# Performance work log

Hardware: AMD Instinct MI355X
Metric: run time of the kernel (lower is better)

## Reference

```python
import jax, jax.numpy as jnp
import numpy as np

N_QUBITS = 10
BATCH = 16384
Q_DEPTH = 2


def _apply_1q_shared(state, U, q):
    # state: [B, 2, 2, ..., 2]; U: [2, 2] complex, acting on wire q
    state = jnp.moveaxis(state, 1 + q, -1)
    state = jnp.einsum('b...i,ji->b...j', state, U)
    return jnp.moveaxis(state, -1, 1 + q)


def _apply_ry_batched(state, angles, q):
    # per-sample RY(angle) on wire q; angles: [B] float
    c = jnp.cos(angles * 0.5).astype(jnp.complex64)
    s = jnp.sin(angles * 0.5).astype(jnp.complex64)
    U = jnp.stack([jnp.stack([c, -s], -1), jnp.stack([s, c], -1)], -2)  # [B,2,2]
    state = jnp.moveaxis(state, 1 + q, -1)
    state = jnp.einsum('b...i,bji->b...j', state, U)
    return jnp.moveaxis(state, -1, 1 + q)


def _rot_matrix(phi, theta, omega):
    # PennyLane Rot = RZ(omega) @ RY(theta) @ RZ(phi)
    c = jnp.cos(theta * 0.5)
    s = jnp.sin(theta * 0.5)
    m00 = jnp.exp(-0.5j * (phi + omega)) * c
    m01 = -jnp.exp(0.5j * (phi - omega)) * s
    m10 = jnp.exp(-0.5j * (phi - omega)) * s
    m11 = jnp.exp(0.5j * (phi + omega)) * c
    return jnp.stack([jnp.stack([m00, m01]), jnp.stack([m10, m11])]).astype(jnp.complex64)


def _apply_cnot(state, c, t):
    st = jnp.moveaxis(state, (1 + c, 1 + t), (1, 2))  # [B, ctrl, tgt, ...]
    st = jnp.stack([st[:, 0], st[:, 1, ::-1]], axis=1)  # flip target where ctrl=1
    return jnp.moveaxis(st, (1, 2), (1 + c, 1 + t))


def setup_inputs() -> dict:
    key = jax.random.key(0)
    k1, k2 = jax.random.split(key)
    x = jax.random.uniform(k1, (BATCH, N_QUBITS), dtype=jnp.float32) * np.pi
    q_weights = 0.01 * jax.random.normal(k2, (Q_DEPTH, N_QUBITS, 3), dtype=jnp.float32)
    return {"x": x, "q_weights": q_weights}


def reference(x, q_weights) -> jnp.ndarray:
    B, n = x.shape
    L = q_weights.shape[0]
    # |0...0> statevector, batched: [B] + [2]*n (axis q <-> wire q, wire 0 most significant)
    state = jnp.zeros((B, 2 ** n), jnp.complex64).at[:, 0].set(1.0)
    state = state.reshape((B,) + (2,) * n)
    # AngleEmbedding(rotation='Y')
    for q in range(n):
        state = _apply_ry_batched(state, x[:, q], q)
    # StronglyEntanglingLayers: Rot on each wire, then ring of CNOTs with range (l % (n-1)) + 1
    for l in range(L):
        for q in range(n):
            U = _rot_matrix(q_weights[l, q, 0], q_weights[l, q, 1], q_weights[l, q, 2])
            state = _apply_1q_shared(state, U, q)
        r = (l % (n - 1)) + 1
        for q in range(n):
            state = _apply_cnot(state, q, (q + r) % n)
    probs = jnp.abs(state.reshape(B, 2 ** n)) ** 2  # [B, 2^n]
    bits = (np.arange(2 ** n)[:, None] >> (n - 1 - np.arange(n))[None, :]) & 1
    signs = jnp.asarray(1.0 - 2.0 * bits, jnp.float32)  # [2^n, n], PauliZ eigenvalues
    return (probs @ signs).astype(jnp.float32)  # [B, n] expvals
```

## Files before the change

### kernel.cpp

```cpp
#include <hip/hip_runtime.h>

#define DEVINL __device__ __forceinline__

struct GC { int laneXor, regXor, rowL, rowR; };
struct Circ { GC g[20]; int sgnL[10], sgnR[10]; };

constexpr Circ build_circ() {
    Circ c{};
    unsigned A[10] = {};
    for (int i = 0; i < 10; ++i) A[i] = 1u << i;
    for (int w = 0; w < 10; ++w) {
        int pos = 9 - w;
        unsigned m = 1u << pos;
        c.g[w] = GC{ int(m >> 4), int(m & 15u), int(m >> 4), int(m & 15u) };
    }
    for (int q = 0; q < 10; ++q) { int pc = 9 - q, pt = 9 - ((q + 1) % 10); A[pt] ^= A[pc]; }
    unsigned M[10] = {}, Inv[10] = {};
    for (int i = 0; i < 10; ++i) { M[i] = A[i]; Inv[i] = 1u << i; }
    for (int col = 0; col < 10; ++col) {
        int piv = col;
        while (!((M[piv] >> col) & 1u)) ++piv;
        unsigned tm = M[col]; M[col] = M[piv]; M[piv] = tm;
        unsigned ti = Inv[col]; Inv[col] = Inv[piv]; Inv[piv] = ti;
        for (int r = 0; r < 10; ++r)
            if (r != col && ((M[r] >> col) & 1u)) { M[r] ^= M[col]; Inv[r] ^= Inv[col]; }
    }
    for (int w = 0; w < 10; ++w) {
        int pos = 9 - w;
        unsigned m = 0;
        for (int i = 0; i < 10; ++i) m |= ((Inv[i] >> pos) & 1u) << i;
        unsigned row = A[pos];
        c.g[10 + w] = GC{ int(m >> 4), int(m & 15u), int(row >> 4), int(row & 15u) };
    }
    for (int q = 0; q < 10; ++q) { int pc = 9 - q, pt = 9 - ((q + 2) % 10); A[pt] ^= A[pc]; }
    for (int q = 0; q < 10; ++q) { unsigned row = A[9 - q]; c.sgnL[q] = int(row >> 4); c.sgnR[q] = int(row & 15u); }
    return c;
}

constexpr Circ CC = build_circ();

static_assert(CC.g[10].rowL == 31 && CC.g[10].rowR == 15, "w0 row");
static_assert(CC.g[11].rowL == 48 && CC.g[11].rowR == 0,  "w1 row");
static_assert(CC.g[12].rowL == 56 && CC.g[12].rowR == 0,  "w2 row");
static_assert(CC.g[13].rowL == 60 && CC.g[13].rowR == 0,  "w3 row");
static_assert(CC.g[14].rowL == 62 && CC.g[14].rowR == 0,  "w4 row");
static_assert(CC.g[15].rowL == 63 && CC.g[15].rowR == 0,  "w5 row");
static_assert(CC.g[16].rowL == 63 && CC.g[16].rowR == 8,  "w6 row");
static_assert(CC.g[17].rowL == 63 && CC.g[17].rowR == 12, "w7 row");
static_assert(CC.g[18].rowL == 63 && CC.g[18].rowR == 14, "w8 row");
static_assert(CC.g[19].rowL == 63 && CC.g[19].rowR == 15, "w9 row");

DEVINL float csw(float v, int sw) {
    return __int_as_float(__float_as_int(v) ^ sw);
}

template<int XOR>
DEVINL float lx(float v, int lane) {
    int x = __float_as_int(v);
    int r;
    if constexpr (XOR < 32) r = __builtin_amdgcn_ds_swizzle(x, 0x1F | (XOR << 10));
    else                    r = __builtin_amdgcn_ds_bpermute((lane ^ XOR) << 2, x);
    return __int_as_float(r);
}

DEVINL void wf(const float* sm, float xw, int w,
               float& a0r, float& a0i, float& a1r, float& a1i) {
    float h = 0.5f * xw;
    float s = __sinf(h), c = __cosf(h);
    float m0 = sm[w * 4 + 0], m1 = sm[w * 4 + 1], m2 = sm[w * 4 + 2], m3 = sm[w * 4 + 3];
    a0r =  m0 * c + m2 * s;
    a0i =  m1 * c + m3 * s;
    a1r = -m2 * c + m0 * s;
    a1i =  m3 * c - m1 * s;
}

template<int G>
DEVINL void rygates(float (&ar)[16], float (&ai)[16], const float* sm, int lane,
                    const int (&sw)[10]) {
    if constexpr (G < 20) {
        constexpr GC gc = CC.g[G];
        constexpr int w = G - 10;
        float t  = sm[40 + w * 4 + 1];
        float tt = csw(t, sw[w]);
        float br_[16], bi_[16];
        if constexpr (gc.laneXor == 0) {
            #pragma unroll
            for (int r = 0; r < 16; ++r) { br_[r] = ar[r ^ gc.regXor]; bi_[r] = ai[r ^ gc.regXor]; }
        } else {
            #pragma unroll
            for (int r = 0; r < 16; ++r) {
                br_[r] = lx<gc.laneXor>(ar[r ^ gc.regXor], lane);
                bi_[r] = lx<gc.laneXor>(ai[r ^ gc.regXor], lane);
            }
        }
        #pragma unroll
        for (int r = 0; r < 16; ++r) {
            const bool sR = __builtin_popcount(unsigned(gc.rowR & r)) & 1;
            if (sR) { ar[r] = fmaf( tt, br_[r], ar[r]); ai[r] = fmaf( tt, bi_[r], ai[r]); }
            else    { ar[r] = fmaf(-tt, br_[r], ar[r]); ai[r] = fmaf(-tt, bi_[r], ai[r]); }
        }
        rygates<G + 1>(ar, ai, sm, lane, sw);
    }
}

__global__ __launch_bounds__(256) void qsim(const float* __restrict__ x,
                                            const float* __restrict__ qw,
                                            float* __restrict__ out, int B) {
    __shared__ float sm[80];
    {
        int g = threadIdx.x;
        if (g < 10) {
            float phi = qw[g * 3 + 0], th = qw[g * 3 + 1], om = qw[g * 3 + 2];
            float c = cosf(0.5f * th), s = sinf(0.5f * th);
            float apo = 0.5f * (phi + om), amo = 0.5f * (phi - om);
            sm[g * 4 + 0] =  cosf(apo) * c;
            sm[g * 4 + 1] = -sinf(apo) * c;
            sm[g * 4 + 2] = -cosf(amo) * s;
            sm[g * 4 + 3] = -sinf(amo) * s;
        } else if (g < 20) {
            int w = g - 10;
            float phi = qw[g * 3 + 0], th = qw[g * 3 + 1];
            float c = cosf(0.5f * th), s = sinf(0.5f * th);
            sm[40 + w * 4 + 0] = c;
            sm[40 + w * 4 + 1] = s / c;
            sm[40 + w * 4 + 2] = cosf(0.5f * phi);
            sm[40 + w * 4 + 3] = -sinf(0.5f * phi);
        }
    }
    __syncthreads();

    int lane = threadIdx.x & 63;
    int b = __builtin_amdgcn_readfirstlane(blockIdx.x * 4 + (threadIdx.x >> 6));
    if (b >= B) return;
    const float* xb = x + b * 10;

    int l = lane;
    int p48 = (l >> 4) ^ (l >> 5);
    int p56 = p48 ^ (l >> 3);
    int p60 = p56 ^ (l >> 2);
    int p62 = p60 ^ (l >> 1);
    int p63 = p62 ^ l;
    int p31 = p63 ^ (l >> 5);
    int s48 = p48 << 31, s56 = p56 << 31, s60 = p60 << 31;
    int s62 = p62 << 31, s63 = p63 << 31, s31 = p31 << 31;
    int sw[10] = { s31, s48, s56, s60, s62, s63, s63, s63, s63, s63 };

    float t01r[4], t01i[4], t23r[4], t23i[4];
    {
        float a0r, a0i, a1r, a1i, b0r, b0i, b1r, b1i;
        wf(sm, xb[9], 9, a0r, a0i, a1r, a1i);
        wf(sm, xb[8], 8, b0r, b0i, b1r, b1i);
        t01r[0] = a0r * b0r - a0i * b0i;  t01i[0] = a0r * b0i + a0i * b0r;
        t01r[1] = a1r * b0r - a1i * b0i;  t01i[1] = a1r * b0i + a1i * b0r;
        t01r[2] = a0r * b1r - a0i * b1i;  t01i[2] = a0r * b1i + a0i * b1r;
        t01r[3] = a1r * b1r - a1i * b1i;  t01i[3] = a1r * b1i + a1i * b1r;
        wf(sm, xb[7], 7, a0r, a0i, a1r, a1i);
        wf(sm, xb[6], 6, b0r, b0i, b1r, b1i);
        t23r[0] = a0r * b0r - a0i * b0i;  t23i[0] = a0r * b0i + a0i * b0r;
        t23r[1] = a1r * b0r - a1i * b0i;  t23i[1] = a1r * b0i + a1i * b0r;
        t23r[2] = a0r * b1r - a0i * b1i;  t23i[2] = a0r * b1i + a0i * b1r;
        t23r[3] = a1r * b1r - a1i * b1i;  t23i[3] = a1r * b1i + a1i * b1r;
    }

    float lfr, lfi;
    {
        float ear = sm[40 + 1 * 4 + 2], eai = csw(sm[40 + 1 * 4 + 3], sw[1]);
        #pragma unroll
        for (int w = 2; w <= 5; ++w) {
            float er = sm[40 + w * 4 + 2], ei = csw(sm[40 + w * 4 + 3], sw[w]);
            float nr = ear * er - eai * ei;
            float ni = ear * ei + eai * er;
            ear = nr; eai = ni;
        }
        float sc = sm[40];
        #pragma unroll
        for (int w = 1; w < 10; ++w) sc *= sm[40 + w * 4];
        lfr = ear * sc; lfi = eai * sc;
        #pragma unroll
        for (int jj = 0; jj < 6; ++jj) {
            int w = 5 - jj;
            float a0r, a0i, a1r, a1i;
            wf(sm, xb[w], w, a0r, a0i, a1r, a1i);
            int bit = (lane >> jj) & 1;
            float pr = bit ? a1r : a0r;
            float pi = bit ? a1i : a0i;
            float nr = lfr * pr - lfi * pi;
            float ni = lfr * pi + lfi * pr;
            lfr = nr; lfi = ni;
        }
    }

    float e6r = sm[40 + 6 * 4 + 2], e6i = csw(sm[40 + 6 * 4 + 3], sw[6]);
    float e7r = sm[40 + 7 * 4 + 2], e7i = csw(sm[40 + 7 * 4 + 3], sw[7]);
    float Pr_ = e6r * e7r - e6i * e7i, Pi_ = e6r * e7i + e6i * e7r;
    float Qr_ = e6r * e7r + e6i * e7i, Qi_ = e6i * e7r - e6r * e7i;
    float t23pr[4], t23pi[4];
    t23pr[0] = t23r[0] * Pr_ - t23i[0] * Pi_;  t23pi[0] = t23r[0] * Pi_ + t23i[0] * Pr_;
    t23pr[1] = t23r[1] * Qr_ - t23i[1] * Qi_;  t23pi[1] = t23r[1] * Qi_ + t23i[1] * Qr_;
    t23pr[2] = t23r[2] * Pr_ + t23i[2] * Pi_;  t23pi[2] = t23i[2] * Pr_ - t23r[2] * Pi_;
    t23pr[3] = t23r[3] * Qr_ + t23i[3] * Qi_;  t23pi[3] = t23i[3] * Qr_ - t23r[3] * Qi_;

    float e0r = sm[40 + 0 * 4 + 2], e0i = csw(sm[40 + 0 * 4 + 3], sw[0]);
    float e9r = sm[40 + 9 * 4 + 2], e9i = csw(sm[40 + 9 * 4 + 3], sw[9]);
    float e8r = sm[40 + 8 * 4 + 2], e8i = csw(sm[40 + 8 * 4 + 3], sw[8]);
    float ebr = e0r * e9r - e0i * e9i, ebi = e0r * e9i + e0i * e9r;
    float G0r = e8r * ebr - e8i * ebi, G0i = e8r * ebi + e8i * ebr;
    float G1r = e8r * ebr + e8i * ebi, G1i = e8i * ebr - e8r * ebi;

    float g4r[4], g4i[4];
    #pragma unroll
    for (int v = 0; v < 4; ++v) {
        g4r[v] = lfr * t01r[v] - lfi * t01i[v];
        g4i[v] = lfr * t01i[v] + lfi * t01r[v];
    }
    float ar[16], ai[16];
    #pragma unroll
    for (int r = 0; r < 16; ++r) {
        float tr = g4r[r & 3] * t23pr[r >> 2] - g4i[r & 3] * t23pi[r >> 2];
        float ti = g4r[r & 3] * t23pi[r >> 2] + g4i[r & 3] * t23pr[r >> 2];
        float gr = (r & 1) ? G1r : G0r;
        float gi = (r & 1) ? G1i : G0i;
        if (__builtin_popcount(unsigned(r & 14)) & 1) gi = -gi;
        ar[r] = tr * gr - ti * gi;
        ai[r] = tr * gi + ti * gr;
    }

    rygates<10>(ar, ai, sm, lane, sw);

    float wv[16];
    #pragma unroll
    for (int r = 0; r < 16; ++r) wv[r] = ar[r] * ar[r] + ai[r] * ai[r];
    #pragma unroll
    for (int bS = 1; bS < 16; bS <<= 1) {
        #pragma unroll
        for (int r = 0; r < 16; ++r) {
            if (!(r & bS)) {
                float xv = wv[r], yv = wv[r | bS];
                wv[r]      = xv + yv;
                wv[r | bS] = xv - yv;
            }
        }
    }

    float e[10];
    #pragma unroll
    for (int q = 0; q < 10; ++q) {
        int slq = __popc(unsigned(lane & CC.sgnL[q])) & 1;
        e[q] = csw(wv[CC.sgnR[q]], slq << 31);
    }
    #pragma unroll
    for (int q = 0; q < 10; ++q) {
        e[q] += lx<1>(e[q], lane);
        e[q] += lx<2>(e[q], lane);
        e[q] += lx<4>(e[q], lane);
        e[q] += lx<8>(e[q], lane);
        e[q] += lx<16>(e[q], lane);
        e[q] += lx<32>(e[q], lane);
    }
    float v = e[0];
    #pragma unroll
    for (int q = 1; q < 10; ++q) v = (lane == q) ? e[q] : v;
    if (lane < 10) out[b * 10 + lane] = v;
}

extern "C" void kernel_launch(void* const* d_in, const int* in_sizes, int n_in,
                              void* d_out, int out_size, void* d_ws, size_t ws_size,
                              hipStream_t stream) {
    const float* x  = (const float*)d_in[0];
    const float* qw = (const float*)d_in[1];
    float* out = (float*)d_out;
    int B = in_sizes[0] / 10;
    int blocks = (B + 3) / 4;
    hipLaunchKernelGGL(qsim, dim3(blocks), dim3(256), 0, stream, x, qw, out, B);
}
```

Baseline: 91.06 us.

## Split weight prep into separate kernel, use DPP/permlane shuffles and packed gate math

Moves the per-block trig precomputation of weight-derived constants into a tiny prep kernel writing a global constant table, removing the shared-memory setup and block barrier from the main kernel. Replaces ds_swizzle/bpermute cross-lane exchanges with DPP quad permutes and permlane16/32 swaps where available. Packs real/imag amplitudes into 2-wide float vectors for packed FMA, reorders the RY gate applications, and trims the final Walsh transform and wave reduction by packing the ten outputs into grouped lanes. It adds a second kernel launch and relies on global-memory constant loads instead of LDS.

```diff
diff --git a/kernel.cpp b/kernel.cpp
--- a/kernel.cpp
+++ b/kernel.cpp
@@ -1,6 +1,8 @@
 #include <hip/hip_runtime.h>
 
 #define DEVINL __device__ __forceinline__
+
+typedef float f32x2 __attribute__((ext_vector_type(2)));
 
 struct GC { int laneXor, regXor, rowL, rowR; };
 struct Circ { GC g[20]; int sgnL[10], sgnR[10]; };
@@ -49,86 +51,136 @@
 static_assert(CC.g[17].rowL == 63 && CC.g[17].rowR == 12, "w7 row");
 static_assert(CC.g[18].rowL == 63 && CC.g[18].rowR == 14, "w8 row");
 static_assert(CC.g[19].rowL == 63 && CC.g[19].rowR == 15, "w9 row");
+static_assert(CC.g[10].laneXor == 48 && CC.g[10].regXor == 0, "w0 m");
+static_assert(CC.g[11].laneXor == 24 && CC.g[12].laneXor == 12, "w1/w2 m");
+static_assert(CC.g[13].laneXor == 6  && CC.g[14].laneXor == 3,  "w3/w4 m");
+static_assert(CC.g[15].laneXor == 1  && CC.g[15].regXor == 8,   "w5 m");
+static_assert(CC.g[16].laneXor == 0 && CC.g[16].regXor == 12, "w6 m");
+static_assert(CC.g[17].laneXor == 0 && CC.g[17].regXor == 6,  "w7 m");
+static_assert(CC.g[18].laneXor == 0 && CC.g[18].regXor == 3,  "w8 m");
+static_assert(CC.g[19].laneXor == 48 && CC.g[19].regXor == 1,   "w9 m");
+
+#if __has_builtin(__builtin_amdgcn_permlane32_swap)
+#define HAS_PL32 1
+#else
+#define HAS_PL32 0
+#endif
+#if __has_builtin(__builtin_amdgcn_permlane16_swap)
+#define HAS_PL16 1
+#else
+#define HAS_PL16 0
+#endif
 
 DEVINL float csw(float v, int sw) {
     return __int_as_float(__float_as_int(v) ^ sw);
 }
 
+DEVINL float xor32_val(float v, int lane) {
+#if HAS_PL32
+    auto r = __builtin_amdgcn_permlane32_swap(__float_as_int(v), __float_as_int(v), false, false);
+    return (__int_as_float(r[0]) + __int_as_float(r[1])) - v;
+#else
+    return __int_as_float(__builtin_amdgcn_ds_bpermute((lane ^ 32) << 2, __float_as_int(v)));
+#endif
+}
+DEVINL float xor48_val(float v, int lane) {
+#if HAS_PL32 && HAS_PL16
+    float t = xor32_val(v, lane);
+    auto r = __builtin_amdgcn_permlane16_swap(__float_as_int(t), __float_as_int(t), false, false);
+    return (__int_as_float(r[0]) + __int_as_float(r[1])) - t;
+#else
+    return __int_as_float(__builtin_amdgcn_ds_bpermute((lane ^ 48) << 2, __float_as_int(v)));
+#endif
+}
+DEVINL float bsum16(float v, int lane) {
+#if HAS_PL16
+    auto r = __builtin_amdgcn_permlane16_swap(__float_as_int(v), __float_as_int(v), false, false);
+    return __int_as_float(r[0]) + __int_as_float(r[1]);
+#else
+    return v + __int_as_float(__builtin_amdgcn_ds_swizzle(__float_as_int(v), 0x1F | (16 << 10)));
+#endif
+}
+DEVINL float bsum32(float v, int lane) {
+#if HAS_PL32
+    auto r = __builtin_amdgcn_permlane32_swap(__float_as_int(v), __float_as_int(v), false, false);
+    return __int_as_float(r[0]) + __int_as_float(r[1]);
+#else
+    return v + __int_as_float(__builtin_amdgcn_ds_bpermute((lane ^ 32) << 2, __float_as_int(v)));
+#endif
+}
+
 template<int XOR>
-DEVINL float lx(float v, int lane) {
-    int x = __float_as_int(v);
-    int r;
-    if constexpr (XOR < 32) r = __builtin_amdgcn_ds_swizzle(x, 0x1F | (XOR << 10));
-    else                    r = __builtin_amdgcn_ds_bpermute((lane ^ XOR) << 2, x);
-    return __int_as_float(r);
-}
-
-DEVINL void wf(const float* sm, float xw, int w,
+DEVINL float fetch(float v, int lane) {
+    if constexpr (XOR == 0)      return v;
+    else if constexpr (XOR == 1) return __int_as_float(__builtin_amdgcn_update_dpp(0, __float_as_int(v), 0xB1, 0xF, 0xF, true));
+    else if constexpr (XOR == 2) return __int_as_float(__builtin_amdgcn_update_dpp(0, __float_as_int(v), 0x4E, 0xF, 0xF, true));
+    else if constexpr (XOR == 3) return __int_as_float(__builtin_amdgcn_update_dpp(0, __float_as_int(v), 0x1B, 0xF, 0xF, true));
+    else if constexpr (XOR == 32) return xor32_val(v, lane);
+    else if constexpr (XOR == 48) return xor48_val(v, lane);
+    else if constexpr (XOR < 32) return __int_as_float(__builtin_amdgcn_ds_swizzle(__float_as_int(v), 0x1F | (XOR << 10)));
+    else return __int_as_float(__builtin_amdgcn_ds_bpermute((lane ^ XOR) << 2, __float_as_int(v)));
+}
+
+__device__ __attribute__((aligned(16))) float g_cst[80];
+
+__global__ void qprep(const float* __restrict__ qw) {
+    int g = threadIdx.x;
+    if (g < 10) {
+        float phi = qw[g * 3 + 0], th = qw[g * 3 + 1], om = qw[g * 3 + 2];
+        float c = cosf(0.5f * th), s = sinf(0.5f * th);
+        float apo = 0.5f * (phi + om), amo = 0.5f * (phi - om);
+        g_cst[g * 4 + 0] =  cosf(apo) * c;
+        g_cst[g * 4 + 1] = -sinf(apo) * c;
+        g_cst[g * 4 + 2] = -cosf(amo) * s;
+        g_cst[g * 4 + 3] = -sinf(amo) * s;
+    } else if (g < 20) {
+        int w = g - 10;
+        float phi = qw[g * 3 + 0], th = qw[g * 3 + 1];
+        float c = cosf(0.5f * th), s = sinf(0.5f * th);
+        g_cst[40 + w] = s / c;
+        g_cst[50 + w * 2 + 0] =  cosf(0.5f * phi);
+        g_cst[50 + w * 2 + 1] = -sinf(0.5f * phi);
+    } else if (g == 20) {
+        float p = 1.f;
+        for (int w = 0; w < 10; ++w) p *= cosf(0.5f * qw[(10 + w) * 3 + 1]);
+        g_cst[70] = p;
+    }
+}
+
+DEVINL void wf(const float* cst, float xw, int w,
                float& a0r, float& a0i, float& a1r, float& a1i) {
     float h = 0.5f * xw;
     float s = __sinf(h), c = __cosf(h);
-    float m0 = sm[w * 4 + 0], m1 = sm[w * 4 + 1], m2 = sm[w * 4 + 2], m3 = sm[w * 4 + 3];
+    float m0 = cst[w * 4 + 0], m1 = cst[w * 4 + 1], m2 = cst[w * 4 + 2], m3 = cst[w * 4 + 3];
     a0r =  m0 * c + m2 * s;
     a0i =  m1 * c + m3 * s;
     a1r = -m2 * c + m0 * s;
     a1i =  m3 * c - m1 * s;
 }
 
-template<int G>
-DEVINL void rygates(float (&ar)[16], float (&ai)[16], const float* sm, int lane,
-                    const int (&sw)[10]) {
-    if constexpr (G < 20) {
-        constexpr GC gc = CC.g[G];
-        constexpr int w = G - 10;
-        float t  = sm[40 + w * 4 + 1];
-        float tt = csw(t, sw[w]);
-        float br_[16], bi_[16];
-        if constexpr (gc.laneXor == 0) {
-            #pragma unroll
-            for (int r = 0; r < 16; ++r) { br_[r] = ar[r ^ gc.regXor]; bi_[r] = ai[r ^ gc.regXor]; }
-        } else {
-            #pragma unroll
-            for (int r = 0; r < 16; ++r) {
-                br_[r] = lx<gc.laneXor>(ar[r ^ gc.regXor], lane);
-                bi_[r] = lx<gc.laneXor>(ai[r ^ gc.regXor], lane);
-            }
-        }
-        #pragma unroll
-        for (int r = 0; r < 16; ++r) {
-            const bool sR = __builtin_popcount(unsigned(gc.rowR & r)) & 1;
-            if (sR) { ar[r] = fmaf( tt, br_[r], ar[r]); ai[r] = fmaf( tt, bi_[r], ai[r]); }
-            else    { ar[r] = fmaf(-tt, br_[r], ar[r]); ai[r] = fmaf(-tt, bi_[r], ai[r]); }
-        }
-        rygates<G + 1>(ar, ai, sm, lane, sw);
+template<int W>
+DEVINL void apply_gate(f32x2 (&a2)[16], const float* cst, int lane, const int (&sw)[10]) {
+    constexpr GC gc = CC.g[10 + W];
+    float tt = csw(cst[40 + W], sw[W]);
+    f32x2 tv; tv.x = tt; tv.y = tt;
+    f32x2 b2[16];
+    #pragma unroll
+    for (int r = 0; r < 16; ++r) {
+        f32x2 s = a2[r ^ gc.regXor];
+        b2[r].x = fetch<gc.laneXor>(s.x, lane);
+        b2[r].y = fetch<gc.laneXor>(s.y, lane);
+    }
+    #pragma unroll
+    for (int r = 0; r < 16; ++r) {
+        const bool sR = __builtin_popcount(unsigned(gc.rowR & r)) & 1;
+        if (sR) a2[r] = a2[r] + tv * b2[r];
+        else    a2[r] = a2[r] - tv * b2[r];
     }
 }
 
 __global__ __launch_bounds__(256) void qsim(const float* __restrict__ x,
-                                            const float* __restrict__ qw,
                                             float* __restrict__ out, int B) {
-    __shared__ float sm[80];
-    {
-        int g = threadIdx.x;
-        if (g < 10) {
-            float phi = qw[g * 3 + 0], th = qw[g * 3 + 1], om = qw[g * 3 + 2];
-            float c = cosf(0.5f * th), s = sinf(0.5f * th);
-            float apo = 0.5f * (phi + om), amo = 0.5f * (phi - om);
-            sm[g * 4 + 0] =  cosf(apo) * c;
-            sm[g * 4 + 1] = -sinf(apo) * c;
-            sm[g * 4 + 2] = -cosf(amo) * s;
-            sm[g * 4 + 3] = -sinf(amo) * s;
-        } else if (g < 20) {
-            int w = g - 10;
-            float phi = qw[g * 3 + 0], th = qw[g * 3 + 1];
-            float c = cosf(0.5f * th), s = sinf(0.5f * th);
-            sm[40 + w * 4 + 0] = c;
-            sm[40 + w * 4 + 1] = s / c;
-            sm[40 + w * 4 + 2] = cosf(0.5f * phi);
-            sm[40 + w * 4 + 3] = -sinf(0.5f * phi);
-        }
-    }
-    __syncthreads();
-
+    const float* cst = g_cst;
     int lane = threadIdx.x & 63;
     int b = __builtin_amdgcn_readfirstlane(blockIdx.x * 4 + (threadIdx.x >> 6));
     if (b >= B) return;
@@ -148,14 +200,14 @@
     float t01r[4], t01i[4], t23r[4], t23i[4];
     {
         float a0r, a0i, a1r, a1i, b0r, b0i, b1r, b1i;
-        wf(sm, xb[9], 9, a0r, a0i, a1r, a1i);
-        wf(sm, xb[8], 8, b0r, b0i, b1r, b1i);
+        wf(cst, xb[9], 9, a0r, a0i, a1r, a1i);
+        wf(cst, xb[8], 8, b0r, b0i, b1r, b1i);
         t01r[0] = a0r * b0r - a0i * b0i;  t01i[0] = a0r * b0i + a0i * b0r;
         t01r[1] = a1r * b0r - a1i * b0i;  t01i[1] = a1r * b0i + a1i * b0r;
         t01r[2] = a0r * b1r - a0i * b1i;  t01i[2] = a0r * b1i + a0i * b1r;
         t01r[3] = a1r * b1r - a1i * b1i;  t01i[3] = a1r * b1i + a1i * b1r;
-        wf(sm, xb[7], 7, a0r, a0i, a1r, a1i);
-        wf(sm, xb[6], 6, b0r, b0i, b1r, b1i);
+        wf(cst, xb[7], 7, a0r, a0i, a1r, a1i);
+        wf(cst, xb[6], 6, b0r, b0i, b1r, b1i);
         t23r[0] = a0r * b0r - a0i * b0i;  t23i[0] = a0r * b0i + a0i * b0r;
         t23r[1] = a1r * b0r - a1i * b0i;  t23i[1] = a1r * b0i + a1i * b0r;
         t23r[2] = a0r * b1r - a0i * b1i;  t23i[2] = a0r * b1i + a0i * b1r;
@@ -164,23 +216,21 @@
 
     float lfr, lfi;
     {
-        float ear = sm[40 + 1 * 4 + 2], eai = csw(sm[40 + 1 * 4 + 3], sw[1]);
+        float ear = cst[50 + 1 * 2], eai = csw(cst[50 + 1 * 2 + 1], sw[1]);
         #pragma unroll
         for (int w = 2; w <= 5; ++w) {
-            float er = sm[40 + w * 4 + 2], ei = csw(sm[40 + w * 4 + 3], sw[w]);
+            float er = cst[50 + w * 2], ei = csw(cst[50 + w * 2 + 1], sw[w]);
             float nr = ear * er - eai * ei;
             float ni = ear * ei + eai * er;
             ear = nr; eai = ni;
         }
-        float sc = sm[40];
-        #pragma unroll
-        for (int w = 1; w < 10; ++w) sc *= sm[40 + w * 4];
+        float sc = cst[70];
         lfr = ear * sc; lfi = eai * sc;
         #pragma unroll
         for (int jj = 0; jj < 6; ++jj) {
             int w = 5 - jj;
             float a0r, a0i, a1r, a1i;
-            wf(sm, xb[w], w, a0r, a0i, a1r, a1i);
+            wf(cst, xb[w], w, a0r, a0i, a1r, a1i);
             int bit = (lane >> jj) & 1;
             float pr = bit ? a1r : a0r;
             float pi = bit ? a1i : a0i;
@@ -190,8 +240,8 @@
         }
     }
 
-    float e6r = sm[40 + 6 * 4 + 2], e6i = csw(sm[40 + 6 * 4 + 3], sw[6]);
-    float e7r = sm[40 + 7 * 4 + 2], e7i = csw(sm[40 + 7 * 4 + 3], sw[7]);
+    float e6r = cst[50 + 6 * 2], e6i = csw(cst[50 + 6 * 2 + 1], sw[6]);
+    float e7r = cst[50 + 7 * 2], e7i = csw(cst[50 + 7 * 2 + 1], sw[7]);
     float Pr_ = e6r * e7r - e6i * e7i, Pi_ = e6r * e7i + e6i * e7r;
     float Qr_ = e6r * e7r + e6i * e7i, Qi_ = e6i * e7r - e6r * e7i;
     float t23pr[4], t23pi[4];
@@ -200,9 +250,9 @@
     t23pr[2] = t23r[2] * Pr_ + t23i[2] * Pi_;  t23pi[2] = t23i[2] * Pr_ - t23r[2] * Pi_;
     t23pr[3] = t23r[3] * Qr_ + t23i[3] * Qi_;  t23pi[3] = t23i[3] * Qr_ - t23r[3] * Qi_;
 
-    float e0r = sm[40 + 0 * 4 + 2], e0i = csw(sm[40 + 0 * 4 + 3], sw[0]);
-    float e9r = sm[40 + 9 * 4 + 2], e9i = csw(sm[40 + 9 * 4 + 3], sw[9]);
-    float e8r = sm[40 + 8 * 4 + 2], e8i = csw(sm[40 + 8 * 4 + 3], sw[8]);
+    float e0r = cst[50 + 0 * 2], e0i = csw(cst[50 + 0 * 2 + 1], sw[0]);
+    float e9r = cst[50 + 9 * 2], e9i = csw(cst[50 + 9 * 2 + 1], sw[9]);
+    float e8r = cst[50 + 8 * 2], e8i = csw(cst[50 + 8 * 2 + 1], sw[8]);
     float ebr = e0r * e9r - e0i * e9i, ebi = e0r * e9i + e0i * e9r;
     float G0r = e8r * ebr - e8i * ebi, G0i = e8r * ebi + e8i * ebr;
     float G1r = e8r * ebr + e8i * ebi, G1i = e8i * ebr - e8r * ebi;
@@ -213,7 +263,7 @@
         g4r[v] = lfr * t01r[v] - lfi * t01i[v];
         g4i[v] = lfr * t01i[v] + lfi * t01r[v];
     }
-    float ar[16], ai[16];
+    f32x2 a2[16];
     #pragma unroll
     for (int r = 0; r < 16; ++r) {
         float tr = g4r[r & 3] * t23pr[r >> 2] - g4i[r & 3] * t23pi[r >> 2];
@@ -221,17 +271,26 @@
         float gr = (r & 1) ? G1r : G0r;
         float gi = (r & 1) ? G1i : G0i;
         if (__builtin_popcount(unsigned(r & 14)) & 1) gi = -gi;
-        ar[r] = tr * gr - ti * gi;
-        ai[r] = tr * gi + ti * gr;
-    }
-
-    rygates<10>(ar, ai, sm, lane, sw);
+        a2[r].x = tr * gr - ti * gi;
+        a2[r].y = tr * gi + ti * gr;
+    }
+
+    apply_gate<1>(a2, cst, lane, sw);
+    apply_gate<4>(a2, cst, lane, sw);
+    apply_gate<2>(a2, cst, lane, sw);
+    apply_gate<5>(a2, cst, lane, sw);
+    apply_gate<3>(a2, cst, lane, sw);
+    apply_gate<6>(a2, cst, lane, sw);
+    apply_gate<0>(a2, cst, lane, sw);
+    apply_gate<7>(a2, cst, lane, sw);
+    apply_gate<9>(a2, cst, lane, sw);
+    apply_gate<8>(a2, cst, lane, sw);
 
     float wv[16];
     #pragma unroll
-    for (int r = 0; r < 16; ++r) wv[r] = ar[r] * ar[r] + ai[r] * ai[r];
-    #pragma unroll
-    for (int bS = 1; bS < 16; bS <<= 1) {
+    for (int r = 0; r < 16; ++r) wv[r] = a2[r].x * a2[r].x + a2[r].y * a2[r].y;
+    #pragma unroll
+    for (int bS = 1; bS < 8; bS <<= 1) {
         #pragma unroll
         for (int r = 0; r < 16; ++r) {
             if (!(r & bS)) {
@@ -245,22 +304,37 @@
     float e[10];
     #pragma unroll
     for (int q = 0; q < 10; ++q) {
+        const int R = CC.sgnR[q];
+        float num = (R & 8) ? (wv[R ^ 8] - wv[R]) : (wv[R] + wv[R ^ 8]);
         int slq = __popc(unsigned(lane & CC.sgnL[q])) & 1;
-        e[q] = csw(wv[CC.sgnR[q]], slq << 31);
-    }
+        e[q] = csw(num, slq << 31);
+    }
+
     #pragma unroll
     for (int q = 0; q < 10; ++q) {
-        e[q] += lx<1>(e[q], lane);
-        e[q] += lx<2>(e[q], lane);
-        e[q] += lx<4>(e[q], lane);
-        e[q] += lx<8>(e[q], lane);
-        e[q] += lx<16>(e[q], lane);
-        e[q] += lx<32>(e[q], lane);
-    }
-    float v = e[0];
-    #pragma unroll
-    for (int q = 1; q < 10; ++q) v = (lane == q) ? e[q] : v;
-    if (lane < 10) out[b * 10 + lane] = v;
+        e[q] += fetch<1>(e[q], lane);
+        e[q] += fetch<2>(e[q], lane);
+    }
+    int s = lane & 3;
+    bool s1 = (s & 1) != 0, s2 = (s & 2) != 0;
+    float v0 = s1 ? e[1] : e[0];
+    float u0 = s1 ? e[3] : e[2];
+    v0 = s2 ? u0 : v0;
+    float v1 = s1 ? e[5] : e[4];
+    float u1 = s1 ? e[7] : e[6];
+    v1 = s2 ? u1 : v1;
+    float v2 = s1 ? e[9] : e[8];
+
+    v0 += fetch<4>(v0, lane);  v1 += fetch<4>(v1, lane);  v2 += fetch<4>(v2, lane);
+    v0 += fetch<8>(v0, lane);  v1 += fetch<8>(v1, lane);  v2 += fetch<8>(v2, lane);
+    v0 = bsum16(v0, lane);     v1 = bsum16(v1, lane);     v2 = bsum16(v2, lane);
+    v0 = bsum32(v0, lane);     v1 = bsum32(v1, lane);     v2 = bsum32(v2, lane);
+
+    float vo = v0;
+    int hi = lane >> 2;
+    vo = (hi == 1) ? v1 : vo;
+    vo = (hi == 2) ? v2 : vo;
+    if (lane < 10) out[b * 10 + lane] = vo;
 }
 
 extern "C" void kernel_launch(void* const* d_in, const int* in_sizes, int n_in,
@@ -271,5 +345,6 @@
     float* out = (float*)d_out;
     int B = in_sizes[0] / 10;
     int blocks = (B + 3) / 4;
-    hipLaunchKernelGGL(qsim, dim3(blocks), dim3(256), 0, stream, x, qw, out, B);
-}
+    hipLaunchKernelGGL(qprep, dim3(1), dim3(64), 0, stream, qw);
+    hipLaunchKernelGGL(qsim, dim3(blocks), dim3(256), 0, stream, x, out, B);
+}
```

After: 101.1 us. 11.0% more time.
